# Optimization experiments

Measured on AMD Instinct MI355X. Metric: run time of the kernel, lower is better.

The kernel has to match this reference:

```python
import jax, jax.numpy as jnp
import numpy as np

K = 3          # kernel size (3x3 branch of SConv_2d)
STRIDE = 1
PAD = 1
NONCENTER = jnp.array([0, 1, 2, 3, 5, 6, 7, 8])      # drop center (idx 4) before sort
REORDER = jnp.array([0, 1, 2, 3, 8, 4, 5, 6, 7])     # reinsert center in the middle


def setup_inputs() -> dict:
    key = jax.random.key(0)
    k1, k2, k3, k4 = jax.random.split(key, 4)
    B, Cin, H, Wd = 8, 64, 128, 128
    Cout = 128
    x = jax.random.normal(k1, (B, Cin, H, Wd), dtype=jnp.float32)
    Coefficient = jax.random.normal(k2, (K * K, K * K), dtype=jnp.float32)
    W = jax.random.normal(k3, (Cout, Cin, K, K), dtype=jnp.float32) * 0.05
    b = jax.random.normal(k4, (Cout,), dtype=jnp.float32) * 0.05
    return {"x": x, "Coefficient": Coefficient, "W": W, "b": b}


def reference(x, Coefficient, W, b):
    # pad (same=False -> constant padding PAD on all sides)
    xp = jnp.pad(x, ((0, 0), (0, 0), (PAD, PAD), (PAD, PAD)))
    B, C, Hp, Wp = xp.shape
    Ho = (Hp - K) // STRIDE + 1
    Wo = (Wp - K) // STRIDE + 1
    # unfold: patches[b, kh*K+kw, c, h, w] == torch unfold+view+permute layout [B, KH*KW, C, H*W]
    patches = jnp.stack(
        [xp[:, :, i:i + Ho * STRIDE:STRIDE, j:j + Wo * STRIDE:STRIDE]
         for i in range(K) for j in range(K)], axis=1)           # [B, 9, C, Ho, Wo]
    center = patches[:, 4:5]                                      # [B, 1, C, Ho, Wo]
    y = jnp.einsum('bjchw,ij->bichw', patches, Coefficient)       # [B, 9, C, Ho, Wo]
    ys = jnp.sort(y[:, NONCENTER], axis=1)                        # sort 8 non-center taps
    z = jnp.concatenate([ys, center], axis=1)                     # [B, 9, C, Ho, Wo]
    z = z[:, REORDER]
    # view(B, KH, KW, C, H, W).permute(0,3,4,1,5,2) -> [B, C, KH*H, KW*W]
    z = z.reshape(B, K, K, C, Ho, Wo).transpose(0, 3, 4, 1, 5, 2).reshape(B, C, K * Ho, K * Wo)
    out = jax.lax.conv_general_dilated(
        z, W, window_strides=(K, K), padding='VALID',
        dimension_numbers=('NCHW', 'OIHW', 'NCHW'))
    return out + b[None, :, None, None]
```

## Files before the change

### kernel.cpp

```cpp
#include <hip/hip_runtime.h>
#include <hip/hip_bf16.h>


#define B_   8
#define C_   64
#define H_   128
#define W_   128
#define CO_  128
#define K_   576
#define MT   64
#define SROW 600

typedef __attribute__((ext_vector_type(8)))  short  short8;
typedef __attribute__((ext_vector_type(8)))  __bf16 bf16x8;
typedef __attribute__((ext_vector_type(16))) float  f32x16;
typedef __attribute__((ext_vector_type(2)))  float  f32x2;

__device__ __forceinline__ void cswap2(f32x2 &a, f32x2 &b) {
    f32x2 lo = __builtin_elementwise_min(a, b);
    f32x2 hi = __builtin_elementwise_max(a, b);
    a = lo; b = hi;
}

__device__ __forceinline__ ushort f2bf(float f) {
    union { float f; unsigned u; } v; v.f = f;
    unsigned r = v.u + 0x7fffu + ((v.u >> 16) & 1u);
    return (ushort)(r >> 16);
}

__device__ __forceinline__ unsigned pack2bf(float lo, float hi) {
    union { __hip_bfloat162 h; unsigned u; } cv;
    cv.h = __float22bfloat162_rn(make_float2(lo, hi));
    return cv.u;
}

__global__ __launch_bounds__(256) void conv_W_bf16(const float* __restrict__ Wg,
                                                   ushort* __restrict__ Wb) {
    int i = blockIdx.x * 256 + threadIdx.x;
    if (i >= CO_ * K_) return;
    const int e    = i & 7;
    const int lane = (i >> 3) & 63;
    const int t    = i >> 9;
    const int nt   = t / 36;
    const int ks   = t - nt * 36;
    const int co   = nt * 32 + (lane & 31);
    const int k    = ks * 16 + (lane >> 5) * 8 + e;
    Wb[i] = f2bf(Wg[co * K_ + k]);
}

__global__ __launch_bounds__(512, 4) void sconv_mfma(
    const float* __restrict__ x,
    const float* __restrict__ Coef,
    const ushort* __restrict__ Wb,
    const float* __restrict__ bias,
    float* __restrict__ out)
{
    __shared__ __align__(16) ushort Zl[MT * SROW];

    const int tid = threadIdx.x;
    const int bx  = blockIdx.x;
    const int wq  = bx & 7;
    const int hq  = (bx >> 3) & 31;
    const int b   = bx >> 8;
    const int w0  = wq * 16;
    const int h0  = hq * 4;

    const int wave = tid >> 6;
    const int lane = tid & 63;
    const int mt   = wave >> 2;
    const int nt   = wave & 3;
    const int r31  = lane & 31;
    const int u    = lane >> 5;
    const ushort* bptr = Wb + ((size_t)(nt * 36) * 64 + lane) * 8;

    {
        const int j  = (tid >> 3) & 7;
        const int c  = wave + 8 * j;
        const int pw = tid & 7;
        const int w  = w0 + pw * 2;
        const float* xb = x + ((size_t)(b * C_ + c)) * (H_ * W_);

        float r[6][4];
        const bool interior = (h0 >= 4) && (h0 <= 120) && (w0 >= 16) && (w0 <= 96);
        if (interior) {
            const float* bp = xb + (h0 - 1) * W_ + (w - 1);
            #pragma unroll
            for (int dy = 0; dy < 6; ++dy) {
                float4 v; __builtin_memcpy(&v, bp + dy * W_, 16);
                r[dy][0] = v.x; r[dy][1] = v.y; r[dy][2] = v.z; r[dy][3] = v.w;
            }
        } else {
            const int wm = w - 1;
            const int wc = min(max(wm, 0), W_ - 4);
            const int s  = wm - wc;
            #pragma unroll
            for (int dy = 0; dy < 6; ++dy) {
                const int hy  = h0 + dy - 1;
                const bool hok = (unsigned)hy < (unsigned)H_;
                const int hc  = min(max(hy, 0), H_ - 1);
                float4 v; __builtin_memcpy(&v, xb + hc * W_ + wc, 16);
                const float rr0 = (s < 0) ? 0.f : ((s > 0) ? v.y : v.x);
                const float rr1 = (s < 0) ? v.x : ((s > 0) ? v.z : v.y);
                const float rr2 = (s < 0) ? v.y : ((s > 0) ? v.w : v.z);
                const float rr3 = (s < 0) ? v.z : ((s > 0) ? 0.f : v.w);
                r[dy][0] = hok ? rr0 : 0.f;
                r[dy][1] = hok ? rr1 : 0.f;
                r[dy][2] = hok ? rr2 : 0.f;
                r[dy][3] = hok ? rr3 : 0.f;
            }
        }

        const int k0 = c * 9;
        const int sw = pw << 4;
        #pragma unroll
        for (int hl = 0; hl < 4; ++hl) {
            f32x2 p2[9];
            #pragma unroll
            for (int dy = 0; dy < 3; ++dy)
                #pragma unroll
                for (int dx = 0; dx < 3; ++dx)
                    p2[dy * 3 + dx] = (f32x2){ r[hl + dy][dx], r[hl + dy][dx + 1] };

            f32x2 v2[8];
            #pragma unroll
            for (int ii = 0; ii < 8; ++ii) {
                const int i = ii + (ii >> 2);
                f32x2 acc = p2[0] * Coef[i * 9];
                #pragma unroll
                for (int jj = 1; jj < 9; ++jj) acc += p2[jj] * Coef[i * 9 + jj];
                v2[ii] = acc;
            }

            cswap2(v2[0],v2[1]); cswap2(v2[2],v2[3]); cswap2(v2[4],v2[5]); cswap2(v2[6],v2[7]);
            cswap2(v2[0],v2[2]); cswap2(v2[1],v2[3]); cswap2(v2[4],v2[6]); cswap2(v2[5],v2[7]);
            cswap2(v2[1],v2[2]); cswap2(v2[5],v2[6]);
            cswap2(v2[0],v2[4]); cswap2(v2[1],v2[5]); cswap2(v2[2],v2[6]); cswap2(v2[3],v2[7]);
            cswap2(v2[2],v2[4]); cswap2(v2[3],v2[5]);
            cswap2(v2[1],v2[2]); cswap2(v2[3],v2[4]); cswap2(v2[5],v2[6]);

            f32x2 z2[9] = { v2[0], v2[1], v2[2], v2[3], p2[4],
                            v2[4], v2[5], v2[6], v2[7] };

            char* zb0 = (char*)Zl + (size_t)(hl * 16 + pw * 2) * (SROW * 2);
            char* zb1 = zb0 + SROW * 2;
            if ((k0 & 1) == 0) {
                #pragma unroll
                for (int q = 0; q < 4; ++q) {
                    *(unsigned*)(zb0 + (((k0 + 2*q) * 2) ^ sw)) = pack2bf(z2[2*q][0], z2[2*q+1][0]);
                    *(unsigned*)(zb1 + (((k0 + 2*q) * 2) ^ sw)) = pack2bf(z2[2*q][1], z2[2*q+1][1]);
                }
                *(ushort*)(zb0 + (((k0 + 8) * 2) ^ sw)) = f2bf(z2[8][0]);
                *(ushort*)(zb1 + (((k0 + 8) * 2) ^ sw)) = f2bf(z2[8][1]);
            } else {
                *(ushort*)(zb0 + ((k0 * 2) ^ sw)) = f2bf(z2[0][0]);
                *(ushort*)(zb1 + ((k0 * 2) ^ sw)) = f2bf(z2[0][1]);
                #pragma unroll
                for (int q = 0; q < 4; ++q) {
                    *(unsigned*)(zb0 + (((k0 + 1 + 2*q) * 2) ^ sw)) = pack2bf(z2[1+2*q][0], z2[2+2*q][0]);
                    *(unsigned*)(zb1 + (((k0 + 1 + 2*q) * 2) ^ sw)) = pack2bf(z2[1+2*q][1], z2[2+2*q][1]);
                }
            }
        }
    }

    short8 bq[8];
    #pragma unroll
    for (int i = 0; i < 8; ++i) bq[i] = *(const short8*)(bptr + i * 512);

    __syncthreads();

    const int arow = mt * 32 + r31;
    const char* abase = (const char*)Zl + (size_t)arow * (SROW * 2);
    const int aswz = ((arow >> 1) & 7) << 4;
    const char* pj[4];
    #pragma unroll
    for (int j = 0; j < 4; ++j)
        pj[j] = abase + (((j * 32) | (u * 16)) ^ aswz);

    bf16x8 aq[4];
    #pragma unroll
    for (int i = 0; i < 4; ++i)
        aq[i] = *(const bf16x8*)(pj[i & 3] + (i >> 2) * 128);

    f32x16 acc = {};

    #pragma unroll
    for (int ks = 0; ks < 36; ++ks) {
        bf16x8 a  = aq[ks & 3];
        short8 bb = bq[ks & 7];
        if (ks + 4 < 36)
            aq[ks & 3] = *(const bf16x8*)(pj[(ks + 4) & 3] + ((ks + 4) >> 2) * 128);
        if (ks + 8 < 36)
            bq[ks & 7] = *(const short8*)(bptr + (ks + 8) * 512);
        acc = __builtin_amdgcn_mfma_f32_32x32x16_bf16(a, __builtin_bit_cast(bf16x8, bb), acc, 0, 0, 0);
    }

    const int co = nt * 32 + r31;
    const float bv = bias[co];
    float* obase = out + (((size_t)(b * CO_ + co)) * H_ + h0 + mt * 2) * W_ + w0;
    #pragma unroll
    for (int qq = 0; qq < 4; ++qq) {
        const int roff = qq * 8 + u * 4;
        const int hl   = roff >> 4;
        const int wl   = roff & 15;
        float4 vv = make_float4(acc[qq*4+0] + bv, acc[qq*4+1] + bv,
                                acc[qq*4+2] + bv, acc[qq*4+3] + bv);
        *(float4*)(obase + hl * W_ + wl) = vv;
    }
}

#define WT 16
__device__ __forceinline__ void cswap(float &a, float &b) {
    float lo = fminf(a, b);
    float hi = fmaxf(a, b);
    a = lo; b = hi;
}
__global__ __launch_bounds__(256) void sconv_fp32(
    const float* __restrict__ x, const float* __restrict__ Coef,
    const float* __restrict__ Wg, const float* __restrict__ bias,
    float* __restrict__ out)
{
    __shared__ float Cf[81];
    __shared__ float Zl[C_ * 9 * WT];
    const int tid = threadIdx.x;
    const int bx  = blockIdx.x;
    const int wt  = bx & 7;
    const int h   = (bx >> 3) & 127;
    const int b   = bx >> 10;
    const int w0  = wt * WT;
    if (tid < 81) Cf[tid] = Coef[tid];
    __syncthreads();
    for (int task = tid; task < C_ * WT; task += 256) {
        const int c = task >> 4, wl = task & 15, w = w0 + wl;
        const float* xb = x + (b * C_ + c) * H_ * W_;
        float p[9];
        #pragma unroll
        for (int dy = 0; dy < 3; ++dy) {
            const int hy = h + dy - 1; const bool hin = (unsigned)hy < (unsigned)H_;
            #pragma unroll
            for (int dx = 0; dx < 3; ++dx) {
                const int wx = w + dx - 1; const bool win = (unsigned)wx < (unsigned)W_;
                p[dy * 3 + dx] = (hin && win) ? xb[hy * W_ + wx] : 0.0f;
            }
        }
        float v[8];
        #pragma unroll
        for (int ii = 0; ii < 8; ++ii) {
            const int i = ii + (ii >> 2);
            float acc = 0.0f;
            #pragma unroll
            for (int j = 0; j < 9; ++j) acc = fmaf(Cf[i * 9 + j], p[j], acc);
            v[ii] = acc;
        }
        cswap(v[0], v[1]); cswap(v[2], v[3]); cswap(v[4], v[5]); cswap(v[6], v[7]);
        cswap(v[0], v[2]); cswap(v[1], v[3]); cswap(v[4], v[6]); cswap(v[5], v[7]);
        cswap(v[1], v[2]); cswap(v[5], v[6]);
        cswap(v[0], v[4]); cswap(v[1], v[5]); cswap(v[2], v[6]); cswap(v[3], v[7]);
        cswap(v[2], v[4]); cswap(v[3], v[5]);
        cswap(v[1], v[2]); cswap(v[3], v[4]); cswap(v[5], v[6]);
        const int base = c * 9 * WT + wl;
        Zl[base + 0*WT]=v[0]; Zl[base + 1*WT]=v[1]; Zl[base + 2*WT]=v[2]; Zl[base + 3*WT]=v[3];
        Zl[base + 4*WT]=p[4];
        Zl[base + 5*WT]=v[4]; Zl[base + 6*WT]=v[5]; Zl[base + 7*WT]=v[6]; Zl[base + 8*WT]=v[7];
    }
    __syncthreads();
    const int co = tid >> 1, w0l = (tid & 1) * 8;
    float acc[8];
    #pragma unroll
    for (int i = 0; i < 8; ++i) acc[i] = 0.0f;
    for (int c = 0; c < C_; ++c) {
        #pragma unroll
        for (int t = 0; t < 9; ++t) {
            const float wv = Wg[(co * C_ + c) * 9 + t];
            const float* zp = &Zl[(c * 9 + t) * WT + w0l];
            const float4 za = *(const float4*)zp;
            const float4 zb = *(const float4*)(zp + 4);
            acc[0]=fmaf(za.x,wv,acc[0]); acc[1]=fmaf(za.y,wv,acc[1]);
            acc[2]=fmaf(za.z,wv,acc[2]); acc[3]=fmaf(za.w,wv,acc[3]);
            acc[4]=fmaf(zb.x,wv,acc[4]); acc[5]=fmaf(zb.y,wv,acc[5]);
            acc[6]=fmaf(zb.z,wv,acc[6]); acc[7]=fmaf(zb.w,wv,acc[7]);
        }
    }
    const float bv = bias[co];
    float* op = out + ((b * CO_ + co) * H_ + h) * W_ + w0 + w0l;
    *(float4*)(op)     = make_float4(acc[0]+bv, acc[1]+bv, acc[2]+bv, acc[3]+bv);
    *(float4*)(op + 4) = make_float4(acc[4]+bv, acc[5]+bv, acc[6]+bv, acc[7]+bv);
}

extern "C" void kernel_launch(void* const* d_in, const int* in_sizes, int n_in,
                              void* d_out, int out_size, void* d_ws, size_t ws_size,
                              hipStream_t stream) {
    const float* x    = (const float*)d_in[0];
    const float* Coef = (const float*)d_in[1];
    const float* Wg   = (const float*)d_in[2];
    const float* bias = (const float*)d_in[3];
    float* out = (float*)d_out;

    const size_t need = (size_t)CO_ * K_ * sizeof(ushort);
    if (ws_size >= need) {
        ushort* Wb = (ushort*)d_ws;
        conv_W_bf16<<<(CO_ * K_ + 255) / 256, 256, 0, stream>>>(Wg, Wb);
        sconv_mfma<<<B_ * (H_ / 4) * (W_ / 16), 512, 0, stream>>>(x, Coef, Wb, bias, out);
    } else {
        sconv_fp32<<<B_ * H_ * 8, 256, 0, stream>>>(x, Coef, Wg, bias, out);
    }
}
```

Before: 137.7 us.

## Permute GEMM K dimension so each channel's 8 sorted taps store as one 16-byte write

Reorders the reduction dimension so the eight sorted non-center taps of each channel occupy one contiguous 16-byte chunk, with all center taps grouped at the end, and permutes the bf16 weight layout to match. The LDS writes become one 128-bit store plus one short per row instead of several unaligned 32-bit and 16-bit stores, and the XOR swizzle is replaced by a padded row stride (584). This targets shared-memory store cost and address arithmetic, at the risk of bank conflicts on the MFMA A-operand reads now that the swizzle is gone.

New measurement: 143.7 us. 1.04x slower.

```diff
diff --git a/kernel.cpp b/kernel.cpp
--- a/kernel.cpp
+++ b/kernel.cpp
@@ -9,7 +9,7 @@
 #define CO_  128
 #define K_   576
 #define MT   64
-#define SROW 600
+#define SROW 584
 
 typedef __attribute__((ext_vector_type(8)))  short  short8;
 typedef __attribute__((ext_vector_type(8)))  __bf16 bf16x8;
@@ -40,12 +40,15 @@
     if (i >= CO_ * K_) return;
     const int e    = i & 7;
     const int lane = (i >> 3) & 63;
-    const int t    = i >> 9;
-    const int nt   = t / 36;
-    const int ks   = t - nt * 36;
+    const int t9   = i >> 9;
+    const int nt   = t9 / 36;
+    const int ks   = t9 - nt * 36;
     const int co   = nt * 32 + (lane & 31);
-    const int k    = ks * 16 + (lane >> 5) * 8 + e;
-    Wb[i] = f2bf(Wg[co * K_ + k]);
+    const int kp   = ks * 16 + (lane >> 5) * 8 + e;
+    int c, t;
+    if (kp < 512) { const int rc = kp >> 3; t = kp & 7; c = ((rc & 7) << 3) | (rc >> 3); }
+    else          { c = kp - 512; t = 8; }
+    Wb[i] = f2bf(Wg[co * K_ + c * 9 + t]);
 }
 
 __global__ __launch_bounds__(512, 4) void sconv_mfma(
@@ -110,8 +113,8 @@
             }
         }
 
-        const int k0 = c * 9;
-        const int sw = pw << 4;
+        const int rcb  = (wave * 8 + j) << 4;
+        const int tailb = 1024 + 2 * c;
         #pragma unroll
         for (int hl = 0; hl < 4; ++hl) {
             f32x2 p2[9];
@@ -143,23 +146,14 @@
 
             char* zb0 = (char*)Zl + (size_t)(hl * 16 + pw * 2) * (SROW * 2);
             char* zb1 = zb0 + SROW * 2;
-            if ((k0 & 1) == 0) {
-                #pragma unroll
-                for (int q = 0; q < 4; ++q) {
-                    *(unsigned*)(zb0 + (((k0 + 2*q) * 2) ^ sw)) = pack2bf(z2[2*q][0], z2[2*q+1][0]);
-                    *(unsigned*)(zb1 + (((k0 + 2*q) * 2) ^ sw)) = pack2bf(z2[2*q][1], z2[2*q+1][1]);
-                }
-                *(ushort*)(zb0 + (((k0 + 8) * 2) ^ sw)) = f2bf(z2[8][0]);
-                *(ushort*)(zb1 + (((k0 + 8) * 2) ^ sw)) = f2bf(z2[8][1]);
-            } else {
-                *(ushort*)(zb0 + ((k0 * 2) ^ sw)) = f2bf(z2[0][0]);
-                *(ushort*)(zb1 + ((k0 * 2) ^ sw)) = f2bf(z2[0][1]);
-                #pragma unroll
-                for (int q = 0; q < 4; ++q) {
-                    *(unsigned*)(zb0 + (((k0 + 1 + 2*q) * 2) ^ sw)) = pack2bf(z2[1+2*q][0], z2[2+2*q][0]);
-                    *(unsigned*)(zb1 + (((k0 + 1 + 2*q) * 2) ^ sw)) = pack2bf(z2[1+2*q][1], z2[2+2*q][1]);
-                }
-            }
+            uint4 q0 = make_uint4(pack2bf(z2[0][0], z2[1][0]), pack2bf(z2[2][0], z2[3][0]),
+                                  pack2bf(z2[4][0], z2[5][0]), pack2bf(z2[6][0], z2[7][0]));
+            uint4 q1 = make_uint4(pack2bf(z2[0][1], z2[1][1]), pack2bf(z2[2][1], z2[3][1]),
+                                  pack2bf(z2[4][1], z2[5][1]), pack2bf(z2[6][1], z2[7][1]));
+            *(uint4*)(zb0 + rcb) = q0;
+            *(uint4*)(zb1 + rcb) = q1;
+            *(ushort*)(zb0 + tailb) = f2bf(z2[8][0]);
+            *(ushort*)(zb1 + tailb) = f2bf(z2[8][1]);
         }
     }
 
@@ -170,17 +164,12 @@
     __syncthreads();
 
     const int arow = mt * 32 + r31;
-    const char* abase = (const char*)Zl + (size_t)arow * (SROW * 2);
-    const int aswz = ((arow >> 1) & 7) << 4;
-    const char* pj[4];
-    #pragma unroll
-    for (int j = 0; j < 4; ++j)
-        pj[j] = abase + (((j * 32) | (u * 16)) ^ aswz);
+    const char* abase = (const char*)Zl + (size_t)arow * (SROW * 2) + u * 16;
 
     bf16x8 aq[4];
     #pragma unroll
     for (int i = 0; i < 4; ++i)
-        aq[i] = *(const bf16x8*)(pj[i & 3] + (i >> 2) * 128);
+        aq[i] = *(const bf16x8*)(abase + i * 32);
 
     f32x16 acc = {};
 
@@ -189,7 +178,7 @@
         bf16x8 a  = aq[ks & 3];
         short8 bb = bq[ks & 7];
         if (ks + 4 < 36)
-            aq[ks & 3] = *(const bf16x8*)(pj[(ks + 4) & 3] + ((ks + 4) >> 2) * 128);
+            aq[ks & 3] = *(const bf16x8*)(abase + (ks + 4) * 32);
         if (ks + 8 < 36)
             bq[ks & 7] = *(const short8*)(bptr + (ks + 8) * 512);
         acc = __builtin_amdgcn_mfma_f32_32x32x16_bf16(a, __builtin_bit_cast(bf16x8, bb), acc, 0, 0, 0);
```
